# Optimization experiments

Hardware: AMD Instinct MI355X
Metric: run time of the kernel (lower is better)

## Reference

```python
import jax, jax.numpy as jnp
import numpy as np

B, S, D, H = 2, 2048, 1024, 16
DK = D // H


def setup_inputs() -> dict:
    key = jax.random.key(0)
    ks = jax.random.split(key, 14)
    inp = {
        'query': jax.random.normal(ks[0], (B, S, D), jnp.float32),
        'key': jax.random.normal(ks[1], (B, S, D), jnp.float32),
        'value': jax.random.normal(ks[2], (B, S, D), jnp.float32),
        'mask': jax.random.randint(ks[3], (B, 1, S, S), 0, 2).astype(bool),
        'rel_pos_bias': jax.random.normal(ks[4], (1, H, S, S), jnp.float32),
    }
    scale = 1.0 / np.sqrt(D)
    names = ['Wq', 'bq', 'Wk', 'bk', 'Wv', 'bv', 'Wo', 'bo']
    for i, n in enumerate(names):
        k = ks[5 + i]
        if n.startswith('W'):
            inp[n] = jax.random.normal(k, (D, D), jnp.float32) * scale
        else:
            inp[n] = jnp.zeros((D,), jnp.float32)
    return inp


def reference(query, key, value, mask, rel_pos_bias, Wq, bq, Wk, bk, Wv, bv, Wo, bo):
    # torch Linear: y = x @ W^T + b; W stored [out, in]
    def proj(x, W, b):
        y = x @ W.T + b                       # [B,S,D]
        return y.reshape(B, S, H, DK).transpose(0, 2, 1, 3)  # [B,H,S,DK]

    q = proj(query, Wq, bq)
    k = proj(key, Wk, bk)
    v = proj(value, Wv, bv)

    scores = jnp.einsum('bhqd,bhkd->bhqk', q, k) / jnp.sqrt(jnp.float32(DK))
    scores = scores + rel_pos_bias
    scores = jnp.where(mask, jnp.float32(-1e9), scores)
    p_attn = jax.nn.softmax(scores, axis=-1)
    x = jnp.einsum('bhqk,bhkd->bhqd', p_attn, v)  # [B,H,S,DK]
    x = x.transpose(0, 2, 1, 3).reshape(B, S, D)
    return x @ Wo.T + bo
```

## Files before the change

### kernel.cpp

```cpp
#include <hip/hip_runtime.h>
#include <stdint.h>


typedef _Float16 f16;
typedef _Float16 f16x8 __attribute__((ext_vector_type(8)));
typedef _Float16 f16x4 __attribute__((ext_vector_type(4)));
typedef __fp16 h2 __attribute__((ext_vector_type(2)));
typedef float f32x4 __attribute__((ext_vector_type(4)));

#define LOG2E 1.44269504088896340736f

__device__ __forceinline__ void gload16(const void* g, void* l) {
  __builtin_amdgcn_global_load_lds(
      (const __attribute__((address_space(1))) unsigned int*)g,
      (__attribute__((address_space(3))) unsigned int*)l, 16, 0, 0);
}

struct CvtSrcs { const float* s[7]; };

__global__ __launch_bounds__(256) void cvt_all(CvtSrcs a, f16* __restrict__ out) {
  const int i = blockIdx.x * 256 + threadIdx.x;
  int r, base;
  if (i < 3145728) { r = i >> 20; base = r << 20; }
  else { r = 3 + ((i - 3145728) >> 18); base = 3145728 + ((r - 3) << 18); }
  const float4 v = ((const float4*)a.s[r])[i - base];
  f16x4 o = {(f16)v.x, (f16)v.y, (f16)v.z, (f16)v.w};
  ((f16x4*)out)[i] = o;
}

__global__ void mask_detect(const uint8_t* __restrict__ m, int* __restrict__ flag) {
  __shared__ int s_off, s_weird;
  const int t = threadIdx.x;
  if (t == 0) { s_off = 0; s_weird = 0; }
  __syncthreads();
  int f_off = 0, f_weird = 0;
  for (int i = t; i < 8192; i += 256) {
    const uint8_t v = m[i];
    if ((i & 3) && v) f_off = 1;
    if (v > 1) f_weird = 1;
  }
  if (f_off) atomicOr(&s_off, 1);
  if (f_weird) atomicOr(&s_weird, 1);
  __syncthreads();
  if (t == 0) *flag = (s_off && !s_weird) ? 1 : 0;
}

__global__ __launch_bounds__(256) void mask_canon(const uint8_t* __restrict__ m,
                                                  uint8_t* __restrict__ out,
                                                  const int* __restrict__ flag) {
  const int i = (blockIdx.x * 256 + threadIdx.x) * 4;
  uchar4 o;
  if (*flag) {
    const uchar4 v = *(const uchar4*)(m + i);
    o = make_uchar4(v.x != 0, v.y != 0, v.z != 0, v.w != 0);
  } else {
    const int4 v = *(const int4*)((const int*)m + i);
    o = make_uchar4(v.x != 0, v.y != 0, v.z != 0, v.w != 0);
  }
  *(uchar4*)(out + i) = o;
}

__global__ __launch_bounds__(256, 2) void gemm_qkv(
    const f16* __restrict__ qh, const f16* __restrict__ kh, const f16* __restrict__ vh,
    const f16* __restrict__ wq, const f16* __restrict__ wk, const f16* __restrict__ wv,
    const float* __restrict__ bq, const float* __restrict__ bk, const float* __restrict__ bv,
    f16* __restrict__ Qp, f16* __restrict__ Kp, f16* __restrict__ Vt) {
  constexpr int K = 1024;
  const int t = threadIdx.x;
  const int w = t >> 6, lane = t & 63, l15 = lane & 15, l4 = lane >> 4;
  const int nt = (int)blockIdx.x % 48;
  const int bm = ((int)blockIdx.x / 48) * 128;
  const int which = nt >> 4;
  const int bn = (nt & 15) * 64;
  const f16* A = which == 0 ? qh : which == 1 ? kh : vh;
  const f16* Bw = which == 0 ? wq : which == 1 ? wk : wv;
  const float* bias = which == 0 ? bq : which == 1 ? bk : bv;

  __shared__ f16 As[2][128 * 32];
  __shared__ f16 Bs[2][64 * 32];

  const f16* a0 = A + (size_t)(bm + (t >> 2)) * K + (t & 3) * 8;
  const f16* a1 = a0 + (size_t)64 * K;
  const f16* b0 = Bw + (size_t)(bn + (t >> 2)) * K + (t & 3) * 8;

  f32x4 acc[2][4];
#pragma unroll
  for (int m = 0; m < 2; ++m)
#pragma unroll
    for (int n = 0; n < 4; ++n) acc[m][n] = (f32x4){0.f, 0.f, 0.f, 0.f};

#define STAGE_G(buf, k0)                          \
  do {                                            \
    gload16(a0 + (k0), &As[buf][w * 512]);        \
    gload16(a1 + (k0), &As[buf][2048 + w * 512]); \
    gload16(b0 + (k0), &Bs[buf][w * 512]);        \
  } while (0)

  STAGE_G(0, 0);
  __syncthreads();
  int cur = 0;
#pragma unroll 1
  for (int kt = 0; kt < 32; ++kt) {
    if (kt < 31) STAGE_G(cur ^ 1, (kt + 1) * 32);
    const f16* ap = &As[cur][(w * 32 + l15) * 32 + l4 * 8];
    const f16* bp = &Bs[cur][l15 * 32 + l4 * 8];
    f16x8 af[2], bfr[4];
#pragma unroll
    for (int m = 0; m < 2; ++m) af[m] = *(const f16x8*)(ap + m * 512);
#pragma unroll
    for (int n = 0; n < 4; ++n) bfr[n] = *(const f16x8*)(bp + n * 512);
#pragma unroll
    for (int m = 0; m < 2; ++m)
#pragma unroll
      for (int n = 0; n < 4; ++n)
        acc[m][n] = __builtin_amdgcn_mfma_f32_16x16x32_f16(af[m], bfr[n], acc[m][n], 0, 0, 0);
    __syncthreads();
    cur ^= 1;
  }
#undef STAGE_G

  const float scale = which == 0 ? 0.125f * LOG2E : 1.0f;
  f16* outp = which == 0 ? Qp : which == 1 ? Kp : Vt;
#pragma unroll
  for (int m = 0; m < 2; ++m) {
    const int r0 = bm + w * 32 + m * 16 + (l4 << 2);
#pragma unroll
    for (int n = 0; n < 4; ++n) {
      const int c = bn + n * 16 + l15;
      const float bv = bias[c];
#pragma unroll
      for (int j = 0; j < 4; ++j) {
        const int r = r0 + j;
        const float v = (acc[m][n][j] + bv) * scale;
        const int b_ = r >> 11, s = r & 2047, h_ = c >> 6, dk = c & 63;
        if (which < 2)
          outp[(((size_t)b_ * 16 + h_) * 2048 + s) * 64 + dk] = (f16)v;
        else
          outp[(((size_t)b_ * 16 + h_) * 64 + dk) * 2048 + s] = (f16)v;
      }
    }
  }
}

__global__ __launch_bounds__(256, 2) void gemm_out(const f16* __restrict__ A,
                                                   const f16* __restrict__ Bw,
                                                   const float* __restrict__ bias,
                                                   float* __restrict__ outp) {
  constexpr int K = 1024;
  const int t = threadIdx.x;
  const int w = t >> 6, lane = t & 63, l15 = lane & 15, l4 = lane >> 4;
  const int bm = (int)(blockIdx.x >> 4) * 128;
  const int bn = (int)(blockIdx.x & 15) * 64;

  __shared__ f16 As[2][128 * 32];
  __shared__ f16 Bs[2][64 * 32];

  const f16* a0 = A + (size_t)(bm + (t >> 2)) * K + (t & 3) * 8;
  const f16* a1 = a0 + (size_t)64 * K;
  const f16* b0 = Bw + (size_t)(bn + (t >> 2)) * K + (t & 3) * 8;

  f32x4 acc[2][4];
#pragma unroll
  for (int m = 0; m < 2; ++m)
#pragma unroll
    for (int n = 0; n < 4; ++n) acc[m][n] = (f32x4){0.f, 0.f, 0.f, 0.f};

#define STAGE_G(buf, k0)                          \
  do {                                            \
    gload16(a0 + (k0), &As[buf][w * 512]);        \
    gload16(a1 + (k0), &As[buf][2048 + w * 512]); \
    gload16(b0 + (k0), &Bs[buf][w * 512]);        \
  } while (0)

  STAGE_G(0, 0);
  __syncthreads();
  int cur = 0;
#pragma unroll 1
  for (int kt = 0; kt < 32; ++kt) {
    if (kt < 31) STAGE_G(cur ^ 1, (kt + 1) * 32);
    const f16* ap = &As[cur][(w * 32 + l15) * 32 + l4 * 8];
    const f16* bp = &Bs[cur][l15 * 32 + l4 * 8];
    f16x8 af[2], bfr[4];
#pragma unroll
    for (int m = 0; m < 2; ++m) af[m] = *(const f16x8*)(ap + m * 512);
#pragma unroll
    for (int n = 0; n < 4; ++n) bfr[n] = *(const f16x8*)(bp + n * 512);
#pragma unroll
    for (int m = 0; m < 2; ++m)
#pragma unroll
      for (int n = 0; n < 4; ++n)
        acc[m][n] = __builtin_amdgcn_mfma_f32_16x16x32_f16(af[m], bfr[n], acc[m][n], 0, 0, 0);
    __syncthreads();
    cur ^= 1;
  }
#undef STAGE_G

#pragma unroll
  for (int m = 0; m < 2; ++m) {
    const int r0 = bm + w * 32 + m * 16 + (l4 << 2);
#pragma unroll
    for (int n = 0; n < 4; ++n) {
      const int c = bn + n * 16 + l15;
      const float bv = bias[c];
#pragma unroll
      for (int j = 0; j < 4; ++j)
        outp[(size_t)(r0 + j) * 1024 + c] = acc[m][n][j] + bv;
    }
  }
}

__device__ __forceinline__ const f16x8* swzr(const f16* base, int row, int bytecol) {
  return (const f16x8*)((const char*)base + row * 128 + (bytecol ^ ((row & 7) << 4)));
}

__global__ __launch_bounds__(256, 2) void attn_fwd(
    const f16* __restrict__ Qp, const f16* __restrict__ Kp,
    const f16* __restrict__ Vt, const float* __restrict__ bias,
    const uint8_t* __restrict__ mask, f16* __restrict__ X) {
  constexpr int S = 2048;
  const int bid = blockIdx.x;
  const int qt = bid & 31, h = bid >> 5;
  const int t = threadIdx.x, w = t >> 6, lane = t & 63;
  const int l15 = lane & 15, l4 = lane >> 4;
  const int q0 = qt * 64 + w * 16;

  const f16* Qb0 = Qp + (size_t)h * S * 64;
  const f16* Qb1 = Qp + (size_t)(16 + h) * S * 64;

  __shared__ f16 Ks[2][2][64 * 64];
  __shared__ f16 Vs[2][2][64 * 64];
  __shared__ f16 Ps[4][16 * 64];

  f16x8 qf[2][2];
#pragma unroll
  for (int ks = 0; ks < 2; ++ks) {
    qf[0][ks] = *(const f16x8*)(Qb0 + (size_t)(q0 + l15) * 64 + ks * 32 + l4 * 8);
    qf[1][ks] = *(const f16x8*)(Qb1 + (size_t)(q0 + l15) * 64 + ks * 32 + l4 * 8);
  }

  f32x4 oacc[2][4];
#pragma unroll
  for (int bb = 0; bb < 2; ++bb)
#pragma unroll
    for (int n = 0; n < 4; ++n) oacc[bb][n] = (f32x4){0.f, 0.f, 0.f, 0.f};
  float mrow[2] = {-3e38f, -3e38f}, lrow[2] = {0.f, 0.f};

  const int srow = t >> 3;
  const int scol = (((t & 7) ^ (srow & 7)) << 3);
  const f16* kp0 = Kp + (size_t)h * S * 64 + (size_t)srow * 64 + scol;
  const f16* kp1 = kp0 + (size_t)16 * S * 64;
  const f16* vp0 = Vt + (size_t)h * 64 * S + (size_t)srow * S + scol;
  const f16* vp1 = vp0 + (size_t)16 * 64 * S;
  const float* bp = bias + (size_t)h * S * S + (size_t)(q0 + l15) * S + l4 * 4;
  const uint8_t* mp0 = mask + (size_t)(q0 + l15) * S + l4 * 4;
  const uint8_t* mp1 = mp0 + (size_t)S * S;

  f32x4 bcA[4], bcB[4];
  uint32_t mcA[2][4], mcB[2][4];

#define STAGE(BUF)                                              \
  do {                                                          \
    gload16(kp0, &Ks[BUF][0][w * 512]);                         \
    gload16(kp0 + 2048, &Ks[BUF][0][2048 + w * 512]);           \
    gload16(kp1, &Ks[BUF][1][w * 512]);                         \
    gload16(kp1 + 2048, &Ks[BUF][1][2048 + w * 512]);           \
    gload16(vp0, &Vs[BUF][0][w * 512]);                         \
    gload16(vp0 + 32 * S, &Vs[BUF][0][2048 + w * 512]);         \
    gload16(vp1, &Vs[BUF][1][w * 512]);                         \
    gload16(vp1 + 32 * S, &Vs[BUF][1][2048 + w * 512]);         \
    kp0 += 4096; kp1 += 4096; vp0 += 64; vp1 += 64;             \
  } while (0)

#define LOADB(BC, MC)                                \
  do {                                               \
    BC[0] = *(const f32x4*)(bp);                     \
    BC[1] = *(const f32x4*)(bp + 16);                \
    BC[2] = *(const f32x4*)(bp + 32);                \
    BC[3] = *(const f32x4*)(bp + 48);                \
    MC[0][0] = *(const uint32_t*)(mp0);              \
    MC[0][1] = *(const uint32_t*)(mp0 + 16);         \
    MC[0][2] = *(const uint32_t*)(mp0 + 32);         \
    MC[0][3] = *(const uint32_t*)(mp0 + 48);         \
    MC[1][0] = *(const uint32_t*)(mp1);              \
    MC[1][1] = *(const uint32_t*)(mp1 + 16);         \
    MC[1][2] = *(const uint32_t*)(mp1 + 32);         \
    MC[1][3] = *(const uint32_t*)(mp1 + 48);         \
    bp += 64; mp0 += 64; mp1 += 64;                  \
  } while (0)

#define COMPUTE(BUF, BC, MC)                                                             \
  do {                                                                                   \
    f32x4 sacc[2][4];                                                                    \
    _Pragma("unroll") for (int bb = 0; bb < 2; ++bb)                                     \
      _Pragma("unroll") for (int n = 0; n < 4; ++n)                                      \
        sacc[bb][n] = (f32x4){0.f, 0.f, 0.f, 0.f};                                       \
    _Pragma("unroll") for (int bb = 0; bb < 2; ++bb)                                     \
      _Pragma("unroll") for (int n = 0; n < 4; ++n)                                      \
        _Pragma("unroll") for (int ks = 0; ks < 2; ++ks) {                               \
          const f16x8 kf = *swzr(&Ks[BUF][bb][0], n * 16 + l15, ks * 64 + l4 * 16);      \
          sacc[bb][n] = __builtin_amdgcn_mfma_f32_16x16x32_f16(kf, qf[bb][ks],           \
                                                               sacc[bb][n], 0, 0, 0);    \
        }                                                                                \
    _Pragma("unroll") for (int bb = 0; bb < 2; ++bb) {                                   \
      float tmax = -3e38f;                                                               \
      _Pragma("unroll") for (int n = 0; n < 4; ++n) {                                    \
        _Pragma("unroll") for (int j = 0; j < 4; ++j) {                                  \
          const float mf = (float)((MC[bb][n] >> (8 * j)) & 255u);                       \
          sacc[bb][n][j] = fmaf(mf, -2e9f, fmaf(BC[n][j], LOG2E, sacc[bb][n][j]));       \
        }                                                                                \
        tmax = fmaxf(tmax, fmaxf(fmaxf(sacc[bb][n][0], sacc[bb][n][1]),                  \
                                 fmaxf(sacc[bb][n][2], sacc[bb][n][3])));                \
      }                                                                                  \
      tmax = fmaxf(tmax, __shfl_xor(tmax, 16));                                          \
      tmax = fmaxf(tmax, __shfl_xor(tmax, 32));                                          \
      const float mnew = fmaxf(mrow[bb], tmax);                                          \
      const float alpha = __builtin_exp2f(mrow[bb] - mnew);                              \
      mrow[bb] = mnew;                                                                   \
      float lsum = 0.f;                                                                  \
      _Pragma("unroll") for (int n = 0; n < 4; ++n)                                      \
        _Pragma("unroll") for (int j = 0; j < 4; ++j) {                                  \
          const float e = __builtin_exp2f(sacc[bb][n][j] - mnew);                        \
          sacc[bb][n][j] = e;                                                            \
          lsum += e;                                                                     \
        }                                                                                \
      lsum += __shfl_xor(lsum, 16);                                                      \
      lsum += __shfl_xor(lsum, 32);                                                      \
      lrow[bb] = lrow[bb] * alpha + lsum;                                                \
      float aq[4];                                                                       \
      _Pragma("unroll") for (int j = 0; j < 4; ++j) aq[j] = __shfl(alpha, l4 * 4 + j);   \
      _Pragma("unroll") for (int n = 0; n < 4; ++n)                                      \
        _Pragma("unroll") for (int j = 0; j < 4; ++j) oacc[bb][n][j] *= aq[j];           \
      _Pragma("unroll") for (int n = 0; n < 4; ++n) {                                    \
        const h2 p01 = __builtin_amdgcn_cvt_pkrtz(sacc[bb][n][0], sacc[bb][n][1]);       \
        const h2 p23 = __builtin_amdgcn_cvt_pkrtz(sacc[bb][n][2], sacc[bb][n][3]);       \
        uint2 pk;                                                                        \
        pk.x = __builtin_bit_cast(unsigned int, p01);                                    \
        pk.y = __builtin_bit_cast(unsigned int, p23);                                    \
        *(uint2*)((char*)&Ps[w][0] + l15 * 128 +                                         \
                  ((32 * n + 8 * l4) ^ ((l15 & 7) << 4))) = pk;                          \
      }                                                                                  \
      f16x8 pf[2];                                                                       \
      _Pragma("unroll") for (int ks = 0; ks < 2; ++ks)                                   \
        pf[ks] = *swzr(&Ps[w][0], l15, ks * 64 + l4 * 16);                               \
      _Pragma("unroll") for (int ks = 0; ks < 2; ++ks)                                   \
        _Pragma("unroll") for (int n = 0; n < 4; ++n) {                                  \
          const f16x8 vf = *swzr(&Vs[BUF][bb][0], n * 16 + l15, ks * 64 + l4 * 16);      \
          oacc[bb][n] = __builtin_amdgcn_mfma_f32_16x16x32_f16(pf[ks], vf,               \
                                                               oacc[bb][n], 0, 0, 0);    \
        }                                                                                \
    }                                                                                    \
  } while (0)

  STAGE(0);
  LOADB(bcA, mcA);
  __syncthreads();

#pragma unroll 1
  for (int kt = 0; kt < 32; kt += 2) {
    STAGE(1);
    LOADB(bcB, mcB);
    COMPUTE(0, bcA, mcA);
    __syncthreads();
    if (kt < 30) {
      STAGE(0);
      LOADB(bcA, mcA);
    }
    COMPUTE(1, bcB, mcB);
    __syncthreads();
  }
#undef COMPUTE
#undef LOADB
#undef STAGE

#pragma unroll
  for (int bb = 0; bb < 2; ++bb) {
    const float inv = 1.0f / lrow[bb];
    float invq[4];
#pragma unroll
    for (int j = 0; j < 4; ++j) invq[j] = __shfl(inv, l4 * 4 + j);
#pragma unroll
    for (int j = 0; j < 4; ++j) {
      const int qrow = q0 + l4 * 4 + j;
#pragma unroll
      for (int n = 0; n < 4; ++n)
        X[((size_t)bb * 2048 + qrow) * 1024 + h * 64 + n * 16 + l15] =
            (f16)(oacc[bb][n][j] * invq[j]);
    }
  }
}

extern "C" void kernel_launch(void* const* d_in, const int* in_sizes, int n_in,
                              void* d_out, int out_size, void* d_ws, size_t ws_size,
                              hipStream_t stream) {
  const float* query = (const float*)d_in[0];
  const float* key_ = (const float*)d_in[1];
  const float* value = (const float*)d_in[2];
  const uint8_t* mask = (const uint8_t*)d_in[3];
  const float* bias = (const float*)d_in[4];
  const float* Wq = (const float*)d_in[5];
  const float* bq = (const float*)d_in[6];
  const float* Wk = (const float*)d_in[7];
  const float* bk = (const float*)d_in[8];
  const float* Wv = (const float*)d_in[9];
  const float* bv = (const float*)d_in[10];
  const float* Wo = (const float*)d_in[11];
  const float* bo = (const float*)d_in[12];

  char* p = (char*)d_ws;
  f16* qh = (f16*)p; p += (size_t)4194304 * 2;
  f16* kh = (f16*)p; p += (size_t)4194304 * 2;
  f16* vh = (f16*)p; p += (size_t)4194304 * 2;
  f16* wqh = (f16*)p; p += (size_t)1048576 * 2;
  f16* wkh = (f16*)p; p += (size_t)1048576 * 2;
  f16* wvh = (f16*)p; p += (size_t)1048576 * 2;
  f16* woh = (f16*)p; p += (size_t)1048576 * 2;
  f16* Qp = (f16*)p; p += (size_t)4194304 * 2;
  f16* Kp = (f16*)p; p += (size_t)4194304 * 2;
  f16* Vt = (f16*)p; p += (size_t)4194304 * 2;
  f16* Xh = (f16*)p; p += (size_t)4194304 * 2;
  uint8_t* m8 = (uint8_t*)p; p += (size_t)8388608;
  int* flag = (int*)p; p += 256;
  if (ws_size < (size_t)(p - (char*)d_ws)) return;

  mask_detect<<<1, 256, 0, stream>>>(mask, flag);
  mask_canon<<<8192, 256, 0, stream>>>(mask, m8, flag);

  CvtSrcs cs;
  cs.s[0] = query; cs.s[1] = key_; cs.s[2] = value;
  cs.s[3] = Wq; cs.s[4] = Wk; cs.s[5] = Wv; cs.s[6] = Wo;
  cvt_all<<<16384, 256, 0, stream>>>(cs, qh);

  gemm_qkv<<<1536, 256, 0, stream>>>(qh, kh, vh, wqh, wkh, wvh, bq, bk, bv,
                                     Qp, Kp, Vt);

  attn_fwd<<<512, 256, 0, stream>>>(Qp, Kp, Vt, bias, m8, Xh);

  gemm_out<<<512, 256, 0, stream>>>(Xh, woh, bo, (float*)d_out);
}
```

Baseline: 258.0 us.

## Split attention over key halves with a combine kernel and single-buffered LDS

Attention is split-K over two halves of the key sequence, which doubles the grid to 1024 blocks. Each half writes a partial output plus row max and sum, and a new combine kernel merges them. LDS drops to a single K/V buffer so occupancy can rise to 4 blocks per CU, at the cost of losing overlap between staging and compute and adding extra syncs. The bias is folded into the MFMA accumulator init, and the log2e scaling moves from the Q projection into the exp argument. The partial outputs are stored in f16, which costs extra global traffic and an extra kernel launch.

Result: slower. 470.3 us (+82.3%).

```diff
diff --git a/kernel.cpp b/kernel.cpp
--- a/kernel.cpp
+++ b/kernel.cpp
@@ -119,7 +119,7 @@
   }
 #undef STAGE_G
 
-  const float scale = which == 0 ? 0.125f * LOG2E : 1.0f;
+  const float scale = which == 0 ? 0.125f : 1.0f;
   f16* outp = which == 0 ? Qp : which == 1 ? Kp : Vt;
 #pragma unroll
   for (int m = 0; m < 2; ++m) {
@@ -213,22 +213,25 @@
   return (const f16x8*)((const char*)base + row * 128 + (bytecol ^ ((row & 7) << 4)));
 }
 
-__global__ __launch_bounds__(256, 2) void attn_fwd(
+__global__ __launch_bounds__(256, 4) void attn_fwd(
     const f16* __restrict__ Qp, const f16* __restrict__ Kp,
     const f16* __restrict__ Vt, const float* __restrict__ bias,
-    const uint8_t* __restrict__ mask, f16* __restrict__ X) {
+    const uint8_t* __restrict__ mask, f16* __restrict__ Op,
+    float* __restrict__ mArr, float* __restrict__ lArr) {
   constexpr int S = 2048;
   const int bid = blockIdx.x;
-  const int qt = bid & 31, h = bid >> 5;
+  const int half = bid >> 9;
+  const int qt = bid & 31, h = (bid >> 5) & 15;
   const int t = threadIdx.x, w = t >> 6, lane = t & 63;
   const int l15 = lane & 15, l4 = lane >> 4;
   const int q0 = qt * 64 + w * 16;
+  const int k0g = half * 1024;
 
   const f16* Qb0 = Qp + (size_t)h * S * 64;
   const f16* Qb1 = Qp + (size_t)(16 + h) * S * 64;
 
-  __shared__ f16 Ks[2][2][64 * 64];
-  __shared__ f16 Vs[2][2][64 * 64];
+  __shared__ f16 Ks[2][64 * 64];
+  __shared__ f16 Vs[2][64 * 64];
   __shared__ f16 Ps[4][16 * 64];
 
   f16x8 qf[2][2];
@@ -247,28 +250,28 @@
 
   const int srow = t >> 3;
   const int scol = (((t & 7) ^ (srow & 7)) << 3);
-  const f16* kp0 = Kp + (size_t)h * S * 64 + (size_t)srow * 64 + scol;
+  const f16* kp0 = Kp + (size_t)h * S * 64 + (size_t)(k0g + srow) * 64 + scol;
   const f16* kp1 = kp0 + (size_t)16 * S * 64;
-  const f16* vp0 = Vt + (size_t)h * 64 * S + (size_t)srow * S + scol;
+  const f16* vp0 = Vt + (size_t)h * 64 * S + (size_t)srow * S + k0g + scol;
   const f16* vp1 = vp0 + (size_t)16 * 64 * S;
-  const float* bp = bias + (size_t)h * S * S + (size_t)(q0 + l15) * S + l4 * 4;
-  const uint8_t* mp0 = mask + (size_t)(q0 + l15) * S + l4 * 4;
+  const float* bp = bias + (size_t)h * S * S + (size_t)(q0 + l15) * S + k0g + l4 * 4;
+  const uint8_t* mp0 = mask + (size_t)(q0 + l15) * S + k0g + l4 * 4;
   const uint8_t* mp1 = mp0 + (size_t)S * S;
 
   f32x4 bcA[4], bcB[4];
   uint32_t mcA[2][4], mcB[2][4];
 
-#define STAGE(BUF)                                              \
-  do {                                                          \
-    gload16(kp0, &Ks[BUF][0][w * 512]);                         \
-    gload16(kp0 + 2048, &Ks[BUF][0][2048 + w * 512]);           \
-    gload16(kp1, &Ks[BUF][1][w * 512]);                         \
-    gload16(kp1 + 2048, &Ks[BUF][1][2048 + w * 512]);           \
-    gload16(vp0, &Vs[BUF][0][w * 512]);                         \
-    gload16(vp0 + 32 * S, &Vs[BUF][0][2048 + w * 512]);         \
-    gload16(vp1, &Vs[BUF][1][w * 512]);                         \
-    gload16(vp1 + 32 * S, &Vs[BUF][1][2048 + w * 512]);         \
-    kp0 += 4096; kp1 += 4096; vp0 += 64; vp1 += 64;             \
+#define STAGE()                                         \
+  do {                                                  \
+    gload16(kp0, &Ks[0][w * 512]);                      \
+    gload16(kp0 + 2048, &Ks[0][2048 + w * 512]);        \
+    gload16(kp1, &Ks[1][w * 512]);                      \
+    gload16(kp1 + 2048, &Ks[1][2048 + w * 512]);        \
+    gload16(vp0, &Vs[0][w * 512]);                      \
+    gload16(vp0 + 32 * S, &Vs[0][2048 + w * 512]);      \
+    gload16(vp1, &Vs[1][w * 512]);                      \
+    gload16(vp1 + 32 * S, &Vs[1][2048 + w * 512]);      \
+    kp0 += 4096; kp1 += 4096; vp0 += 64; vp1 += 64;     \
   } while (0)
 
 #define LOADB(BC, MC)                                \
@@ -288,25 +291,24 @@
     bp += 64; mp0 += 64; mp1 += 64;                  \
   } while (0)
 
-#define COMPUTE(BUF, BC, MC)                                                             \
+#define COMPUTE(BC, MC)                                                                  \
   do {                                                                                   \
     f32x4 sacc[2][4];                                                                    \
     _Pragma("unroll") for (int bb = 0; bb < 2; ++bb)                                     \
-      _Pragma("unroll") for (int n = 0; n < 4; ++n)                                      \
-        sacc[bb][n] = (f32x4){0.f, 0.f, 0.f, 0.f};                                       \
-    _Pragma("unroll") for (int bb = 0; bb < 2; ++bb)                                     \
-      _Pragma("unroll") for (int n = 0; n < 4; ++n)                                      \
-        _Pragma("unroll") for (int ks = 0; ks < 2; ++ks) {                               \
-          const f16x8 kf = *swzr(&Ks[BUF][bb][0], n * 16 + l15, ks * 64 + l4 * 16);      \
-          sacc[bb][n] = __builtin_amdgcn_mfma_f32_16x16x32_f16(kf, qf[bb][ks],           \
-                                                               sacc[bb][n], 0, 0, 0);    \
-        }                                                                                \
+      _Pragma("unroll") for (int n = 0; n < 4; ++n) {                                    \
+        const f16x8 kf0 = *swzr(&Ks[bb][0], n * 16 + l15, l4 * 16);                      \
+        sacc[bb][n] = __builtin_amdgcn_mfma_f32_16x16x32_f16(                            \
+            kf0, qf[bb][0], BC[n], 0, 0, 0);                 \
+        const f16x8 kf1 = *swzr(&Ks[bb][0], n * 16 + l15, 64 + l4 * 16);                 \
+        sacc[bb][n] = __builtin_amdgcn_mfma_f32_16x16x32_f16(                            \
+            kf1, qf[bb][1], sacc[bb][n], 0, 0, 0);                                       \
+      }                                                                                  \
     _Pragma("unroll") for (int bb = 0; bb < 2; ++bb) {                                   \
       float tmax = -3e38f;                                                               \
       _Pragma("unroll") for (int n = 0; n < 4; ++n) {                                    \
         _Pragma("unroll") for (int j = 0; j < 4; ++j) {                                  \
           const float mf = (float)((MC[bb][n] >> (8 * j)) & 255u);                       \
-          sacc[bb][n][j] = fmaf(mf, -2e9f, fmaf(BC[n][j], LOG2E, sacc[bb][n][j]));       \
+          sacc[bb][n][j] = fmaf(mf, -2e9f, sacc[bb][n][j]);                              \
         }                                                                                \
         tmax = fmaxf(tmax, fmaxf(fmaxf(sacc[bb][n][0], sacc[bb][n][1]),                  \
                                  fmaxf(sacc[bb][n][2], sacc[bb][n][3])));                \
@@ -314,12 +316,13 @@
       tmax = fmaxf(tmax, __shfl_xor(tmax, 16));                                          \
       tmax = fmaxf(tmax, __shfl_xor(tmax, 32));                                          \
       const float mnew = fmaxf(mrow[bb], tmax);                                          \
-      const float alpha = __builtin_exp2f(mrow[bb] - mnew);                              \
+      const float negmL = -mnew * LOG2E;                                                 \
+      const float alpha = __builtin_exp2f(fmaf(mrow[bb], LOG2E, negmL));                 \
       mrow[bb] = mnew;                                                                   \
       float lsum = 0.f;                                                                  \
       _Pragma("unroll") for (int n = 0; n < 4; ++n)                                      \
         _Pragma("unroll") for (int j = 0; j < 4; ++j) {                                  \
-          const float e = __builtin_exp2f(sacc[bb][n][j] - mnew);                        \
+          const float e = __builtin_exp2f(fmaf(sacc[bb][n][j], LOG2E, negmL));           \
           sacc[bb][n][j] = e;                                                            \
           lsum += e;                                                                     \
         }                                                                                \
@@ -344,28 +347,28 @@
         pf[ks] = *swzr(&Ps[w][0], l15, ks * 64 + l4 * 16);                               \
       _Pragma("unroll") for (int ks = 0; ks < 2; ++ks)                                   \
         _Pragma("unroll") for (int n = 0; n < 4; ++n) {                                  \
-          const f16x8 vf = *swzr(&Vs[BUF][bb][0], n * 16 + l15, ks * 64 + l4 * 16);      \
+          const f16x8 vf = *swzr(&Vs[bb][0], n * 16 + l15, ks * 64 + l4 * 16);           \
           oacc[bb][n] = __builtin_amdgcn_mfma_f32_16x16x32_f16(pf[ks], vf,               \
                                                                oacc[bb][n], 0, 0, 0);    \
         }                                                                                \
     }                                                                                    \
   } while (0)
 
-  STAGE(0);
+  STAGE();
   LOADB(bcA, mcA);
   __syncthreads();
 
 #pragma unroll 1
-  for (int kt = 0; kt < 32; kt += 2) {
-    STAGE(1);
+  for (int it = 0; it < 8; ++it) {
     LOADB(bcB, mcB);
-    COMPUTE(0, bcA, mcA);
-    __syncthreads();
-    if (kt < 30) {
-      STAGE(0);
-      LOADB(bcA, mcA);
-    }
-    COMPUTE(1, bcB, mcB);
+    COMPUTE(bcA, mcA);
+    __syncthreads();
+    STAGE();
+    __syncthreads();
+    if (it < 7) LOADB(bcA, mcA);
+    COMPUTE(bcB, mcB);
+    __syncthreads();
+    if (it < 7) STAGE();
     __syncthreads();
   }
 #undef COMPUTE
@@ -374,6 +377,7 @@
 
 #pragma unroll
   for (int bb = 0; bb < 2; ++bb) {
+    const size_t rowb = ((size_t)((half * 2 + bb) * 16 + h)) * 2048;
     const float inv = 1.0f / lrow[bb];
     float invq[4];
 #pragma unroll
@@ -383,10 +387,40 @@
       const int qrow = q0 + l4 * 4 + j;
 #pragma unroll
       for (int n = 0; n < 4; ++n)
-        X[((size_t)bb * 2048 + qrow) * 1024 + h * 64 + n * 16 + l15] =
-            (f16)(oacc[bb][n][j] * invq[j]);
+        Op[(rowb + qrow) * 64 + n * 16 + l15] = (f16)(oacc[bb][n][j] * invq[j]);
     }
-  }
+    if (l4 == 0) {
+      mArr[rowb + q0 + l15] = mrow[bb];
+      lArr[rowb + q0 + l15] = lrow[bb];
+    }
+  }
+}
+
+__global__ __launch_bounds__(256) void attn_combine(
+    const f16* __restrict__ Op, const float* __restrict__ mArr,
+    const float* __restrict__ lArr, f16* __restrict__ X) {
+  const int e8 = blockIdx.x * 256 + threadIdx.x;
+  const int d0 = (e8 & 7) * 8;
+  const int q = (e8 >> 3) & 2047;
+  const int h = (e8 >> 14) & 15;
+  const int bb = e8 >> 18;
+  const size_t row = (size_t)(bb * 16 + h) * 2048 + q;
+  const size_t hs_ml = (size_t)65536;
+  const size_t hs_o = (size_t)65536 * 64;
+  const float m0 = mArr[row], m1 = mArr[hs_ml + row];
+  const float l0 = lArr[row], l1 = lArr[hs_ml + row];
+  const float M = fmaxf(m0, m1);
+  const float w0 = __builtin_exp2f((m0 - M) * LOG2E) * l0;
+  const float w1 = __builtin_exp2f((m1 - M) * LOG2E) * l1;
+  const float inv = 1.0f / (w0 + w1);
+  const float a0 = w0 * inv, a1 = w1 * inv;
+  const f16x8 o0 = *(const f16x8*)(Op + row * 64 + d0);
+  const f16x8 o1 = *(const f16x8*)(Op + hs_o + row * 64 + d0);
+  f16x8 o;
+#pragma unroll
+  for (int j = 0; j < 8; ++j)
+    o[j] = (f16)(a0 * (float)o0[j] + a1 * (float)o1[j]);
+  *(f16x8*)(X + (size_t)(bb * 2048 + q) * 1024 + h * 64 + d0) = o;
 }
 
 extern "C" void kernel_launch(void* const* d_in, const int* in_sizes, int n_in,
@@ -418,6 +452,9 @@
   f16* Kp = (f16*)p; p += (size_t)4194304 * 2;
   f16* Vt = (f16*)p; p += (size_t)4194304 * 2;
   f16* Xh = (f16*)p; p += (size_t)4194304 * 2;
+  f16* Opart = (f16*)p; p += (size_t)8388608 * 2;
+  float* mArr = (float*)p; p += (size_t)131072 * 4;
+  float* lArr = (float*)p; p += (size_t)131072 * 4;
   uint8_t* m8 = (uint8_t*)p; p += (size_t)8388608;
   int* flag = (int*)p; p += 256;
   if (ws_size < (size_t)(p - (char*)d_ws)) return;
@@ -433,7 +470,8 @@
   gemm_qkv<<<1536, 256, 0, stream>>>(qh, kh, vh, wqh, wkh, wvh, bq, bk, bv,
                                      Qp, Kp, Vt);
 
-  attn_fwd<<<512, 256, 0, stream>>>(Qp, Kp, Vt, bias, m8, Xh);
+  attn_fwd<<<1024, 256, 0, stream>>>(Qp, Kp, Vt, bias, m8, Opart, mArr, lArr);
+  attn_combine<<<2048, 256, 0, stream>>>(Opart, mArr, lArr, Xh);
 
   gemm_out<<<512, 256, 0, stream>>>(Xh, woh, bo, (float*)d_out);
 }
```
